# Performance work log

Hardware: AMD Instinct MI355X
Metric: run time of the kernel (lower is better)

## Reference

```python
import jax, jax.numpy as jnp
import numpy as np

N, D_IN, D_KQ, D_V = 4096, 1024, 1024, 1024


def setup_inputs() -> dict:
    key = jax.random.key(0)
    kx, kq, kk, kv = jax.random.split(key, 4)
    return {
        "x": jax.random.normal(kx, (N, D_IN), dtype=jnp.float32),
        "W_query": jax.random.uniform(kq, (D_IN, D_KQ), dtype=jnp.float32),
        "W_key": jax.random.uniform(kk, (D_IN, D_KQ), dtype=jnp.float32),
        "W_value": jax.random.uniform(kv, (D_IN, D_V), dtype=jnp.float32),
        "masked": 1,
    }


def reference(x, W_query, W_key, W_value, masked):
    # x: [N, d_in]; single-head, unbatched attention
    queries = x @ W_query          # [N, d_kq]
    keys = x @ W_key               # [N, d_kq]
    values = x @ W_value           # [N, d_v]
    scores = queries @ keys.T      # [N, N]
    if masked:  # masked is a static Python int
        n = x.shape[0]
        causal = jnp.triu(jnp.ones((n, n), dtype=bool), k=1)
        scores = jnp.where(causal, -jnp.inf, scores)
    scale = 1.0 / jnp.sqrt(jnp.asarray(W_key.shape[1], dtype=scores.dtype))
    attn = jax.nn.softmax(scores * scale, axis=-1)
    return attn @ values           # [N, d_v]
```

## Files before the change

kernel.cpp:

```cpp
#include <hip/hip_runtime.h>
#include <hip/hip_bf16.h>


using bf16 = __hip_bfloat16;
using f32x4 = __attribute__((ext_vector_type(4))) float;
using i32x4 = __attribute__((ext_vector_type(4))) int;
using i8 = signed char;

__device__ __forceinline__ void gload_lds16(const void* g, void* l) {
  __builtin_amdgcn_global_load_lds(
      (const __attribute__((address_space(1))) void*)g,
      (__attribute__((address_space(3))) void*)l, 16, 0, 0);
}

template <int ROWS, int CPR, int NT>
__device__ __forceinline__ void stage_tile8(const i8* __restrict__ g, i8* s,
                                            int ld) {
  const int t = threadIdx.x;
#pragma unroll
  for (int c = 0; c < ROWS * CPR / NT; ++c) {
    const int idx = c * NT + t;
    const int row = idx / CPR;
    const int ch = idx & (CPR - 1);
    const int cg = ch ^ ((row >> 1) & (CPR - 1));
    gload_lds16(g + (size_t)row * ld + cg * 16, s + idx * 16);
  }
}
template <int CPR>
__device__ __forceinline__ i32x4 frag_at8(const i8* s, int row, int ch) {
  return *(const i32x4*)&s[(row * CPR + (ch ^ ((row >> 1) & (CPR - 1)))) * 16];
}

__device__ __forceinline__ i32x4 mfma_i8(i32x4 a, i32x4 b, i32x4 c) {
  return __builtin_amdgcn_mfma_i32_16x16x64_i8(a, b, c, 0, 0, 0);
}

__global__ __launch_bounds__(256, 3) void gemm_qkv_i8(
    const i8* __restrict__ xh, const i8* __restrict__ xl,
    const i8* __restrict__ qTh, const i8* __restrict__ qTl,
    const i8* __restrict__ kTh, const i8* __restrict__ kTl,
    const i8* __restrict__ vTh, const i8* __restrict__ vTl,
    const float* __restrict__ srow, i8* __restrict__ Qh, i8* __restrict__ Ql,
    i8* __restrict__ Kh, i8* __restrict__ Kl, i8* __restrict__ V8) {
  __shared__ __align__(16) i8 sAh[128 * 64], sAl[128 * 64];
  __shared__ __align__(16) i8 sBh[64 * 64], sBl[64 * 64];

  const int bx = blockIdx.x;
  const int which = bx >> 4;
  const int n0 = (bx & 15) * 64;
  const int m0 = blockIdx.y * 128;
  const i8* Bh = which == 0 ? qTh : which == 1 ? kTh : vTh;
  const i8* Bl = which == 0 ? qTl : which == 1 ? kTl : vTl;
  const i8* A_h = xh + (size_t)m0 * 1024;
  const i8* A_l = xl + (size_t)m0 * 1024;
  const i8* B_h = Bh + (size_t)n0 * 1024;
  const i8* B_l = Bl + (size_t)n0 * 1024;

  const int t = threadIdx.x, lane = t & 63, w = t >> 6;
  const int wr = (w >> 1) * 64, wc = (w & 1) * 32;
  const int frow = lane & 15, fc = lane >> 4;

  i32x4 a0[4][2], a1[4][2];
#pragma unroll
  for (int i = 0; i < 4; ++i)
#pragma unroll
    for (int j = 0; j < 2; ++j) {
      a0[i][j] = (i32x4){0, 0, 0, 0};
      a1[i][j] = (i32x4){0, 0, 0, 0};
    }

  for (int kt = 0; kt < 16; ++kt) {
    const int k0 = kt * 64;
    stage_tile8<128, 4, 256>(A_h + k0, sAh, 1024);
    stage_tile8<64, 4, 256>(B_h + k0, sBh, 1024);
    stage_tile8<128, 4, 256>(A_l + k0, sAl, 1024);
    stage_tile8<64, 4, 256>(B_l + k0, sBl, 1024);
    __syncthreads();

    i32x4 ah[4], al[4], bh[2], bl[2];
#pragma unroll
    for (int i = 0; i < 4; ++i) {
      ah[i] = frag_at8<4>(sAh, wr + i * 16 + frow, fc);
      al[i] = frag_at8<4>(sAl, wr + i * 16 + frow, fc);
    }
#pragma unroll
    for (int j = 0; j < 2; ++j) {
      bh[j] = frag_at8<4>(sBh, wc + j * 16 + frow, fc);
      bl[j] = frag_at8<4>(sBl, wc + j * 16 + frow, fc);
    }
#pragma unroll
    for (int i = 0; i < 4; ++i)
#pragma unroll
      for (int j = 0; j < 2; ++j) {
        a0[i][j] = mfma_i8(ah[i], bh[j], a0[i][j]);
        a1[i][j] = mfma_i8(ah[i], bl[j], a1[i][j]);
        a1[i][j] = mfma_i8(al[i], bh[j], a1[i][j]);
      }
    __syncthreads();
  }

  const int er = (lane >> 4) * 4, ec = lane & 15;
  if (which < 2) {
    i8* Ph = which == 0 ? Qh : Kh;
    i8* Pl = which == 0 ? Ql : Kl;
#pragma unroll
    for (int i = 0; i < 4; ++i)
#pragma unroll
      for (int j = 0; j < 2; ++j)
#pragma unroll
        for (int r = 0; r < 4; ++r) {
          const int gm = m0 + wr + i * 16 + er + r;
          const int gn = n0 + wc + j * 16 + ec;
          const float Qf =
              65536.f * (float)a0[i][j][r] + 256.f * (float)a1[i][j][r];
          int q16 = __float2int_rn(Qf * (1.f / 262144.f));
          q16 = min(max(q16, -32511), 32511);
          const int h = (q16 + 128) >> 8;
          const int l = q16 - (h << 8);
          const size_t off = (size_t)gm * 1024 + gn;
          Ph[off] = (i8)h;
          Pl[off] = (i8)l;
        }
  } else {
#pragma unroll
    for (int i = 0; i < 4; ++i)
#pragma unroll
      for (int j = 0; j < 2; ++j)
#pragma unroll
        for (int r = 0; r < 4; ++r) {
          const int gm = m0 + wr + i * 16 + er + r;
          const int gn = n0 + wc + j * 16 + ec;
          const float Vf =
              (65536.f * (float)a0[i][j][r] + 256.f * (float)a1[i][j][r]) *
                  (1.f / 134217728.f) +
              0.5f * srow[gm];
          int v8 = __float2int_rn(Vf);
          v8 = min(max(v8, -127), 127);
          V8[(size_t)gm * 1024 + gn] = (i8)v8;
        }
  }
}

__global__ __launch_bounds__(256, 3) void gemm_s_i8(
    const i8* __restrict__ Qh, const i8* __restrict__ Ql,
    const i8* __restrict__ Kh, const i8* __restrict__ Kl,
    const float* __restrict__ srow, const float* __restrict__ qsum,
    const float* __restrict__ ksum, float* __restrict__ S) {
  const int cb = blockIdx.x, rb = blockIdx.y;
  if (cb > 2 * rb + 1) return;
  const int n0 = cb * 64, m0 = rb * 128;
  __shared__ __align__(16) i8 sAh[128 * 64], sAl[128 * 64];
  __shared__ __align__(16) i8 sBh[64 * 64], sBl[64 * 64];

  const i8* A_h = Qh + (size_t)m0 * 1024;
  const i8* A_l = Ql + (size_t)m0 * 1024;
  const i8* B_h = Kh + (size_t)n0 * 1024;
  const i8* B_l = Kl + (size_t)n0 * 1024;

  const int t = threadIdx.x, lane = t & 63, w = t >> 6;
  const int wr = (w >> 1) * 64, wc = (w & 1) * 32;
  const int frow = lane & 15, fc = lane >> 4;

  i32x4 a0[4][2], a1[4][2];
#pragma unroll
  for (int i = 0; i < 4; ++i)
#pragma unroll
    for (int j = 0; j < 2; ++j) {
      a0[i][j] = (i32x4){0, 0, 0, 0};
      a1[i][j] = (i32x4){0, 0, 0, 0};
    }

  for (int kt = 0; kt < 16; ++kt) {
    const int k0 = kt * 64;
    stage_tile8<128, 4, 256>(A_h + k0, sAh, 1024);
    stage_tile8<64, 4, 256>(B_h + k0, sBh, 1024);
    stage_tile8<128, 4, 256>(A_l + k0, sAl, 1024);
    stage_tile8<64, 4, 256>(B_l + k0, sBl, 1024);
    __syncthreads();

    i32x4 ah[4], al[4], bh[2], bl[2];
#pragma unroll
    for (int i = 0; i < 4; ++i) {
      ah[i] = frag_at8<4>(sAh, wr + i * 16 + frow, fc);
      al[i] = frag_at8<4>(sAl, wr + i * 16 + frow, fc);
    }
#pragma unroll
    for (int j = 0; j < 2; ++j) {
      bh[j] = frag_at8<4>(sBh, wc + j * 16 + frow, fc);
      bl[j] = frag_at8<4>(sBl, wc + j * 16 + frow, fc);
    }
#pragma unroll
    for (int i = 0; i < 4; ++i)
#pragma unroll
      for (int j = 0; j < 2; ++j) {
        a0[i][j] = mfma_i8(ah[i], bh[j], a0[i][j]);
        a1[i][j] = mfma_i8(ah[i], bl[j], a1[i][j]);
        a1[i][j] = mfma_i8(al[i], bh[j], a1[i][j]);
      }
    __syncthreads();
  }

  const int er = (lane >> 4) * 4, ec = lane & 15;
  float sn[2], kn[2];
#pragma unroll
  for (int j = 0; j < 2; ++j) {
    const int gn = n0 + wc + j * 16 + ec;
    sn[j] = srow[gn];
    kn[j] = ksum[gn];
  }
#pragma unroll
  for (int i = 0; i < 4; ++i)
#pragma unroll
    for (int r = 0; r < 4; ++r) {
      const int gm = m0 + wr + i * 16 + er + r;
      const float sm = srow[gm], qm = qsum[gm];
#pragma unroll
      for (int j = 0; j < 2; ++j) {
        const int gn = n0 + wc + j * 16 + ec;
        const float Sf =
            65536.f * (float)a0[i][j][r] + 256.f * (float)a1[i][j][r];
        const float logit = Sf * (1.f / 8388608.f) +
                            0.015625f * (sn[j] * qm + sm * kn[j]) +
                            8.f * sm * sn[j];
        S[(size_t)gm * 4096 + gn] = logit;
      }
    }
}

__global__ __launch_bounds__(256, 4) void gemm_pv_i8(
    const i8* __restrict__ P, const i8* __restrict__ VT,
    const float* __restrict__ inv_s, float* __restrict__ O) {
  __shared__ __align__(16) i8 sP[128 * 64];
  __shared__ __align__(16) i8 sV[64 * 64];

  const int bxr = blockIdx.x;
  const int rb = (bxr & 1) ? (31 - (bxr >> 1)) : (bxr >> 1);
  const int m0 = rb * 128;
  const int n0 = blockIdx.y * 64;
  const int ktiles = 2 * (rb + 1);

  const i8* A0 = P + (size_t)m0 * 4096;
  const i8* B0 = VT + (size_t)n0 * 4096;

  const int t = threadIdx.x, lane = t & 63, w = t >> 6;
  const int wr = (w >> 1) * 64, wc = (w & 1) * 32;
  const int frow = lane & 15, fc = lane >> 4;

  i32x4 a0[4][2];
#pragma unroll
  for (int i = 0; i < 4; ++i)
#pragma unroll
    for (int j = 0; j < 2; ++j) a0[i][j] = (i32x4){0, 0, 0, 0};

  for (int kt = 0; kt < ktiles; ++kt) {
    const int k0 = kt * 64;
    stage_tile8<128, 4, 256>(A0 + k0, sP, 4096);
    stage_tile8<64, 4, 256>(B0 + k0, sV, 4096);
    __syncthreads();

    i32x4 pa[4], b[2];
#pragma unroll
    for (int i = 0; i < 4; ++i) pa[i] = frag_at8<4>(sP, wr + i * 16 + frow, fc);
#pragma unroll
    for (int j = 0; j < 2; ++j) b[j] = frag_at8<4>(sV, wc + j * 16 + frow, fc);
#pragma unroll
    for (int i = 0; i < 4; ++i)
#pragma unroll
      for (int j = 0; j < 2; ++j) a0[i][j] = mfma_i8(pa[i], b[j], a0[i][j]);
    __syncthreads();
  }

  const int er = (lane >> 4) * 4, ec = lane & 15;
#pragma unroll
  for (int i = 0; i < 4; ++i)
#pragma unroll
    for (int j = 0; j < 2; ++j)
#pragma unroll
      for (int r = 0; r < 4; ++r) {
        const int gm = m0 + wr + i * 16 + er + r;
        const int gn = n0 + wc + j * 16 + ec;
        O[(size_t)gm * 1024 + gn] =
            (float)a0[i][j][r] * inv_s[gm] * (1.f / 127.f);
      }
}

__global__ __launch_bounds__(256) void softmax_kernel(
    const float* __restrict__ S, i8* __restrict__ P,
    float* __restrict__ inv_s, int N) {
  const int wid = threadIdx.x >> 6;
  const int r0 = blockIdx.x * 2 + (wid >> 1);
  const int row = (wid & 1) ? (N - 1 - r0) : r0;
  const int lane = threadIdx.x & 63;
  const float* s = S + (size_t)row * N;
  i8* p = P + (size_t)row * N;
  const int len = row + 1;
  const int nv4 = len >> 2;
  const float4* s4 = (const float4*)s;

  float m = -3.4e38f;
  for (int j = lane; j < nv4; j += 64) {
    const float4 v = s4[j];
    m = fmaxf(m, fmaxf(fmaxf(v.x, v.y), fmaxf(v.z, v.w)));
  }
  for (int j = (nv4 << 2) + lane; j < len; j += 64) m = fmaxf(m, s[j]);
#pragma unroll
  for (int off = 32; off > 0; off >>= 1) m = fmaxf(m, __shfl_xor(m, off, 64));

  float sum = 0.f;
  for (int j = lane; j < nv4; j += 64) {
    const float4 v = s4[j];
    const float e0 = __expf(v.x - m), e1 = __expf(v.y - m);
    const float e2 = __expf(v.z - m), e3 = __expf(v.w - m);
    sum += (e0 + e1) + (e2 + e3);
    uint pk = (uint)__float2int_rn(e0 * 127.f);
    pk |= (uint)__float2int_rn(e1 * 127.f) << 8;
    pk |= (uint)__float2int_rn(e2 * 127.f) << 16;
    pk |= (uint)__float2int_rn(e3 * 127.f) << 24;
    *(uint*)(p + 4 * j) = pk;
  }
  for (int j = (nv4 << 2) + lane; j < len; j += 64) {
    const float e = __expf(s[j] - m);
    sum += e;
    p[j] = (i8)__float2int_rn(e * 127.f);
  }
#pragma unroll
  for (int off = 32; off > 0; off >>= 1) sum += __shfl_xor(sum, off, 64);

  const int bound = ((row >> 7) + 1) << 7;
  for (int j = len + lane; j < bound; j += 64) p[j] = (i8)0;
  if (lane == 0) inv_s[row] = 1.f / sum;
}

__global__ void split_x_i8(const float4* __restrict__ x, uint* __restrict__ h,
                           uint* __restrict__ l, int n4) {
  const int i = blockIdx.x * blockDim.x + threadIdx.x;
  if (i >= n4) return;
  const float4 v = x[i];
  const float f[4] = {v.x, v.y, v.z, v.w};
  uint hp = 0, lp = 0;
#pragma unroll
  for (int k = 0; k < 4; ++k) {
    int q = __float2int_rn(f[k] * 4096.f);
    q = min(max(q, -32511), 32511);
    const int hh = (q + 128) >> 8;
    const int ll = q - (hh << 8);
    hp |= (uint)(hh & 255) << (8 * k);
    lp |= (uint)(ll & 255) << (8 * k);
  }
  h[i] = hp;
  l[i] = lp;
}

__global__ void split_transpose_w_i8(
    const float* __restrict__ W0, const float* __restrict__ W1,
    const float* __restrict__ W2, i8* __restrict__ T0h, i8* __restrict__ T0l,
    i8* __restrict__ T1h, i8* __restrict__ T1l, i8* __restrict__ T2h,
    i8* __restrict__ T2l, int R, int C) {
  const int z = blockIdx.z;
  const float* W = z == 0 ? W0 : z == 1 ? W1 : W2;
  i8* Th = z == 0 ? T0h : z == 1 ? T1h : T2h;
  i8* Tl = z == 0 ? T0l : z == 1 ? T1l : T2l;
  __shared__ float tile[32][33];
  const int c0 = blockIdx.x * 32, r0 = blockIdx.y * 32;
  const int tx = threadIdx.x, ty = threadIdx.y;
  for (int rr = ty; rr < 32; rr += 8)
    tile[rr][tx] = W[(size_t)(r0 + rr) * C + c0 + tx];
  __syncthreads();
  for (int cc = ty; cc < 32; cc += 8) {
    const float v = tile[tx][cc] - 0.5f;
    int w16 = __float2int_rn(v * 32768.f);
    w16 = min(max(w16, -32511), 32511);
    const int h = (w16 + 128) >> 8;
    const int l = w16 - (h << 8);
    const size_t off = (size_t)(c0 + cc) * R + r0 + tx;
    Th[off] = (i8)h;
    Tl[off] = (i8)l;
  }
}

__global__ __launch_bounds__(256) void wrow_kernel(const float* __restrict__ Wq,
                                                   const float* __restrict__ Wk,
                                                   float* __restrict__ wqrow,
                                                   float* __restrict__ wkrow) {
  const int k = blockIdx.x * 4 + (threadIdx.x >> 6);
  const int lane = threadIdx.x & 63;
  const float* W = blockIdx.y == 0 ? Wq : Wk;
  float* out = blockIdx.y == 0 ? wqrow : wkrow;
  const float* row = W + (size_t)k * 1024;
  float s = 0.f;
  for (int c = lane; c < 1024; c += 64) s += row[c];
#pragma unroll
  for (int off = 32; off > 0; off >>= 1) s += __shfl_xor(s, off, 64);
  if (lane == 0) out[k] = s - 512.f;
}

__global__ __launch_bounds__(256) void rowstats_kernel(
    const float* __restrict__ x, const float* __restrict__ wqrow,
    const float* __restrict__ wkrow, float* __restrict__ srow,
    float* __restrict__ qsum, float* __restrict__ ksum) {
  const int i = blockIdx.x * 4 + (threadIdx.x >> 6);
  const int lane = threadIdx.x & 63;
  const float* row = x + (size_t)i * 1024;
  float ss = 0.f, sq = 0.f, sk = 0.f;
  for (int c = lane; c < 1024; c += 64) {
    const float v = row[c];
    ss += v;
    sq += v * wqrow[c];
    sk += v * wkrow[c];
  }
#pragma unroll
  for (int off = 32; off > 0; off >>= 1) {
    ss += __shfl_xor(ss, off, 64);
    sq += __shfl_xor(sq, off, 64);
    sk += __shfl_xor(sk, off, 64);
  }
  if (lane == 0) {
    srow[i] = ss;
    qsum[i] = sq;
    ksum[i] = sk;
  }
}

__global__ void transpose_v8(const i8* __restrict__ V8, i8* __restrict__ T,
                             int R, int C) {
  __shared__ i8 tile[32][33];
  const int c0 = blockIdx.x * 32, r0 = blockIdx.y * 32;
  const int tx = threadIdx.x, ty = threadIdx.y;
  for (int rr = ty; rr < 32; rr += 8)
    tile[rr][tx] = V8[(size_t)(r0 + rr) * C + c0 + tx];
  __syncthreads();
  for (int cc = ty; cc < 32; cc += 8)
    T[(size_t)(c0 + cc) * R + r0 + tx] = tile[tx][cc];
}

extern "C" void kernel_launch(void* const* d_in, const int* in_sizes, int n_in,
                              void* d_out, int out_size, void* d_ws,
                              size_t ws_size, hipStream_t stream) {
  (void)in_sizes; (void)n_in; (void)out_size; (void)ws_size;
  const float* x = (const float*)d_in[0];
  const float* Wq = (const float*)d_in[1];
  const float* Wk = (const float*)d_in[2];
  const float* Wv = (const float*)d_in[3];

  const int N = 4096, D = 1024;

  char* p = (char*)d_ws;
  auto alloc = [&](size_t bytes) {
    char* r = p;
    p += (bytes + 255) & ~(size_t)255;
    return r;
  };
  i8* xh = (i8*)alloc((size_t)N * D);
  i8* xl = (i8*)alloc((size_t)N * D);
  i8* WqTh = (i8*)alloc((size_t)D * D);
  i8* WqTl = (i8*)alloc((size_t)D * D);
  i8* WkTh = (i8*)alloc((size_t)D * D);
  i8* WkTl = (i8*)alloc((size_t)D * D);
  i8* WvTh = (i8*)alloc((size_t)D * D);
  i8* WvTl = (i8*)alloc((size_t)D * D);
  i8* Qh = (i8*)alloc((size_t)N * D);
  i8* Ql = (i8*)alloc((size_t)N * D);
  i8* Kh = (i8*)alloc((size_t)N * D);
  i8* Kl = (i8*)alloc((size_t)N * D);
  i8* V8 = (i8*)alloc((size_t)N * D);
  i8* VT = (i8*)alloc((size_t)D * N);
  float* S = (float*)alloc((size_t)N * N * 4);
  i8* P = (i8*)alloc((size_t)N * N);
  float* inv_s = (float*)alloc((size_t)N * 4);
  float* srow = (float*)alloc((size_t)N * 4);
  float* qsum = (float*)alloc((size_t)N * 4);
  float* ksum = (float*)alloc((size_t)N * 4);
  float* wqrow = (float*)alloc((size_t)D * 4);
  float* wkrow = (float*)alloc((size_t)D * 4);

  split_x_i8<<<N * D / 4 / 256, 256, 0, stream>>>((const float4*)x, (uint*)xh,
                                                  (uint*)xl, N * D / 4);
  split_transpose_w_i8<<<dim3(32, 32, 3), dim3(32, 8), 0, stream>>>(
      Wq, Wk, Wv, WqTh, WqTl, WkTh, WkTl, WvTh, WvTl, D, D);
  wrow_kernel<<<dim3(D / 4, 2), 256, 0, stream>>>(Wq, Wk, wqrow, wkrow);
  rowstats_kernel<<<N / 4, 256, 0, stream>>>(x, wqrow, wkrow, srow, qsum, ksum);

  gemm_qkv_i8<<<dim3(48, 32), 256, 0, stream>>>(xh, xl, WqTh, WqTl, WkTh, WkTl,
                                                WvTh, WvTl, srow, Qh, Ql, Kh,
                                                Kl, V8);
  transpose_v8<<<dim3(D / 32, N / 32), dim3(32, 8), 0, stream>>>(V8, VT, N, D);

  gemm_s_i8<<<dim3(64, 32), 256, 0, stream>>>(Qh, Ql, Kh, Kl, srow, qsum, ksum,
                                              S);

  softmax_kernel<<<N / 4, 256, 0, stream>>>(S, P, inv_s, N);

  gemm_pv_i8<<<dim3(32, 16), 256, 0, stream>>>(P, VT, inv_s, (float*)d_out);
}
```

Baseline: 238.8 us.

## Fuse V transpose into QKV epilogue and compute row max in S GEMM

The QKV GEMM epilogue now packs four consecutive rows of the V tile into one 32-bit word and writes V transposed directly, which removes the separate transpose kernel and the V8 buffer. The S GEMM epilogue also computes a per-row maximum over causal entries, encoding the float so that unsigned ordering matches float ordering, and combines it with shuffles and atomicMax into a zero-initialised buffer. The softmax kernel then reads this max instead of making an extra pass over S. The cost is extra atomics and an additional memset, and the transposed 4-byte stores are strided across rows.

```diff
diff --git a/kernel.cpp b/kernel.cpp
--- a/kernel.cpp
+++ b/kernel.cpp
@@ -11,6 +11,14 @@
   __builtin_amdgcn_global_load_lds(
       (const __attribute__((address_space(1))) void*)g,
       (__attribute__((address_space(3))) void*)l, 16, 0, 0);
+}
+
+__device__ __forceinline__ uint f2mono(float f) {
+  const uint b = __float_as_uint(f);
+  return (b & 0x80000000u) ? ~b : (b | 0x80000000u);
+}
+__device__ __forceinline__ float mono2f(uint u) {
+  return __uint_as_float((u & 0x80000000u) ? (u ^ 0x80000000u) : ~u);
 }
 
 template <int ROWS, int CPR, int NT>
@@ -41,7 +49,7 @@
     const i8* __restrict__ kTh, const i8* __restrict__ kTl,
     const i8* __restrict__ vTh, const i8* __restrict__ vTl,
     const float* __restrict__ srow, i8* __restrict__ Qh, i8* __restrict__ Ql,
-    i8* __restrict__ Kh, i8* __restrict__ Kl, i8* __restrict__ V8) {
+    i8* __restrict__ Kh, i8* __restrict__ Kl, i8* __restrict__ VT) {
   __shared__ __align__(16) i8 sAh[128 * 64], sAl[128 * 64];
   __shared__ __align__(16) i8 sBh[64 * 64], sBl[64 * 64];
 
@@ -122,22 +130,27 @@
           Pl[off] = (i8)l;
         }
   } else {
+    const int gm_base = m0 + wr;
 #pragma unroll
     for (int i = 0; i < 4; ++i)
 #pragma unroll
-      for (int j = 0; j < 2; ++j)
+      for (int j = 0; j < 2; ++j) {
+        const int gn = n0 + wc + j * 16 + ec;
+        const float sbase = 0.5f;
+        uint pk = 0;
 #pragma unroll
         for (int r = 0; r < 4; ++r) {
-          const int gm = m0 + wr + i * 16 + er + r;
-          const int gn = n0 + wc + j * 16 + ec;
+          const int gm = gm_base + i * 16 + er + r;
           const float Vf =
               (65536.f * (float)a0[i][j][r] + 256.f * (float)a1[i][j][r]) *
                   (1.f / 134217728.f) +
-              0.5f * srow[gm];
+              sbase * srow[gm];
           int v8 = __float2int_rn(Vf);
           v8 = min(max(v8, -127), 127);
-          V8[(size_t)gm * 1024 + gn] = (i8)v8;
+          pk |= (uint)(v8 & 255) << (8 * r);
         }
+        *(uint*)(VT + (size_t)gn * 4096 + gm_base + i * 16 + er) = pk;
+      }
   }
 }
 
@@ -145,7 +158,8 @@
     const i8* __restrict__ Qh, const i8* __restrict__ Ql,
     const i8* __restrict__ Kh, const i8* __restrict__ Kl,
     const float* __restrict__ srow, const float* __restrict__ qsum,
-    const float* __restrict__ ksum, float* __restrict__ S) {
+    const float* __restrict__ ksum, float* __restrict__ S,
+    uint* __restrict__ rowmax) {
   const int cb = blockIdx.x, rb = blockIdx.y;
   if (cb > 2 * rb + 1) return;
   const int n0 = cb * 64, m0 = rb * 128;
@@ -214,6 +228,7 @@
     for (int r = 0; r < 4; ++r) {
       const int gm = m0 + wr + i * 16 + er + r;
       const float sm = srow[gm], qm = qsum[gm];
+      uint um = 0;
 #pragma unroll
       for (int j = 0; j < 2; ++j) {
         const int gn = n0 + wc + j * 16 + ec;
@@ -223,7 +238,12 @@
                             0.015625f * (sn[j] * qm + sm * kn[j]) +
                             8.f * sm * sn[j];
         S[(size_t)gm * 4096 + gn] = logit;
+        if (gn <= gm) um = max(um, f2mono(logit));
       }
+#pragma unroll
+      for (int msk = 1; msk < 16; msk <<= 1)
+        um = max(um, (uint)__shfl_xor((int)um, msk, 64));
+      if ((lane & 15) == 0) atomicMax(&rowmax[gm], um);
     }
 }
 
@@ -285,8 +305,8 @@
 }
 
 __global__ __launch_bounds__(256) void softmax_kernel(
-    const float* __restrict__ S, i8* __restrict__ P,
-    float* __restrict__ inv_s, int N) {
+    const float* __restrict__ S, const uint* __restrict__ rowmax,
+    i8* __restrict__ P, float* __restrict__ inv_s, int N) {
   const int wid = threadIdx.x >> 6;
   const int r0 = blockIdx.x * 2 + (wid >> 1);
   const int row = (wid & 1) ? (N - 1 - r0) : r0;
@@ -297,14 +317,7 @@
   const int nv4 = len >> 2;
   const float4* s4 = (const float4*)s;
 
-  float m = -3.4e38f;
-  for (int j = lane; j < nv4; j += 64) {
-    const float4 v = s4[j];
-    m = fmaxf(m, fmaxf(fmaxf(v.x, v.y), fmaxf(v.z, v.w)));
-  }
-  for (int j = (nv4 << 2) + lane; j < len; j += 64) m = fmaxf(m, s[j]);
-#pragma unroll
-  for (int off = 32; off > 0; off >>= 1) m = fmaxf(m, __shfl_xor(m, off, 64));
+  const float m = mono2f(rowmax[row]);
 
   float sum = 0.f;
   for (int j = lane; j < nv4; j += 64) {
@@ -421,18 +434,6 @@
   }
 }
 
-__global__ void transpose_v8(const i8* __restrict__ V8, i8* __restrict__ T,
-                             int R, int C) {
-  __shared__ i8 tile[32][33];
-  const int c0 = blockIdx.x * 32, r0 = blockIdx.y * 32;
-  const int tx = threadIdx.x, ty = threadIdx.y;
-  for (int rr = ty; rr < 32; rr += 8)
-    tile[rr][tx] = V8[(size_t)(r0 + rr) * C + c0 + tx];
-  __syncthreads();
-  for (int cc = ty; cc < 32; cc += 8)
-    T[(size_t)(c0 + cc) * R + r0 + tx] = tile[tx][cc];
-}
-
 extern "C" void kernel_launch(void* const* d_in, const int* in_sizes, int n_in,
                               void* d_out, int out_size, void* d_ws,
                               size_t ws_size, hipStream_t stream) {
@@ -462,7 +463,6 @@
   i8* Ql = (i8*)alloc((size_t)N * D);
   i8* Kh = (i8*)alloc((size_t)N * D);
   i8* Kl = (i8*)alloc((size_t)N * D);
-  i8* V8 = (i8*)alloc((size_t)N * D);
   i8* VT = (i8*)alloc((size_t)D * N);
   float* S = (float*)alloc((size_t)N * N * 4);
   i8* P = (i8*)alloc((size_t)N * N);
@@ -472,6 +472,9 @@
   float* ksum = (float*)alloc((size_t)N * 4);
   float* wqrow = (float*)alloc((size_t)D * 4);
   float* wkrow = (float*)alloc((size_t)D * 4);
+  uint* rowmax = (uint*)alloc((size_t)N * 4);
+
+  hipMemsetAsync(rowmax, 0, (size_t)N * 4, stream);
 
   split_x_i8<<<N * D / 4 / 256, 256, 0, stream>>>((const float4*)x, (uint*)xh,
                                                   (uint*)xl, N * D / 4);
@@ -482,13 +485,12 @@
 
   gemm_qkv_i8<<<dim3(48, 32), 256, 0, stream>>>(xh, xl, WqTh, WqTl, WkTh, WkTl,
                                                 WvTh, WvTl, srow, Qh, Ql, Kh,
-                                                Kl, V8);
-  transpose_v8<<<dim3(D / 32, N / 32), dim3(32, 8), 0, stream>>>(V8, VT, N, D);
+                                                Kl, VT);
 
   gemm_s_i8<<<dim3(64, 32), 256, 0, stream>>>(Qh, Ql, Kh, Kl, srow, qsum, ksum,
-                                              S);
-
-  softmax_kernel<<<N / 4, 256, 0, stream>>>(S, P, inv_s, N);
+                                              S, rowmax);
+
+  softmax_kernel<<<N / 4, 256, 0, stream>>>(S, rowmax, P, inv_s, N);
 
   gemm_pv_i8<<<dim3(32, 16), 256, 0, stream>>>(P, VT, inv_s, (float*)d_out);
 }
```

Measured after the change: 246.3 us. 3.2% more time.
